# Kernel tuning notes

Hardware: AMD Instinct MI355X
Metric: run time of the kernel (lower is better)

The kernel has to match this reference:

```python
import jax, jax.numpy as jnp
import numpy as np

N = 512      # num_nodes
B = 32       # batch
T = 12       # encoder seq_len
HOR = 12     # decoder horizon
U = 64       # rnn_units
K = 2        # max_diffusion_step
M = 2 * K + 1  # num_matrices (2 supports)


def setup_inputs() -> dict:
    key = jax.random.key(0)
    ks = jax.random.split(key, 16)

    # dual random-walk supports: (D^-1 A)^T and (D^-1 A^T)^T, with self loops
    adj = (jax.random.uniform(ks[0], (N, N)) < 32.0 / N).astype(jnp.float32)

    def rw_T(a):
        a = a + jnp.eye(N, dtype=jnp.float32)
        return (a / a.sum(axis=1, keepdims=True)).T

    supports = jnp.stack([rw_T(adj), rw_T(adj.T)])  # (2, N, N)

    def w(k, shape, s=0.1):
        return jax.random.normal(k, shape, dtype=jnp.float32) * s

    Cin0 = (1 + U) * M   # layer0: input_dim(1)+units, times num_matrices
    Cin1 = (U + U) * M   # layer1
    return {
        "inputs": jax.random.normal(ks[1], (T, B, N * 1), dtype=jnp.float32),
        "supports": supports,
        "enc0_Wg": w(ks[2], (Cin0, 2 * U)), "enc0_bg": jnp.ones(2 * U, jnp.float32),
        "enc0_Wc": w(ks[3], (Cin0, U)),     "enc0_bc": jnp.zeros(U, jnp.float32),
        "enc1_Wg": w(ks[4], (Cin1, 2 * U)), "enc1_bg": jnp.ones(2 * U, jnp.float32),
        "enc1_Wc": w(ks[5], (Cin1, U)),     "enc1_bc": jnp.zeros(U, jnp.float32),
        "dec0_Wg": w(ks[6], (Cin0, 2 * U)), "dec0_bg": jnp.ones(2 * U, jnp.float32),
        "dec0_Wc": w(ks[7], (Cin0, U)),     "dec0_bc": jnp.zeros(U, jnp.float32),
        "dec1_Wg": w(ks[8], (Cin1, 2 * U)), "dec1_bg": jnp.ones(2 * U, jnp.float32),
        "dec1_Wc": w(ks[9], (Cin1, U)),     "dec1_bc": jnp.zeros(U, jnp.float32),
        "proj_W": w(ks[10], (U, 1)),        "proj_b": jnp.zeros(1, jnp.float32),
    }


def reference(inputs, supports, enc0_Wg, enc0_bg, enc0_Wc, enc0_bc,
              enc1_Wg, enc1_bg, enc1_Wc, enc1_bc,
              dec0_Wg, dec0_bg, dec0_Wc, dec0_bc,
              dec1_Wg, dec1_bg, dec1_Wc, dec1_bc, proj_W, proj_b):
    Bsz = inputs.shape[1]

    def gconv(x0, W, b):
        # x0: (B, N, C); Chebyshev-style diffusion over each support
        xs = [x0]
        for i in range(supports.shape[0]):
            s = supports[i]
            x1 = jnp.einsum('ij,bjc->bic', s, x0)
            xs.append(x1)
            xp, xpp = x1, x0
            for _ in range(K - 1):
                x2 = 2.0 * jnp.einsum('ij,bjc->bic', s, xp) - xpp
                xs.append(x2)
                xp, xpp = x2, xp
        # stack on last axis to match torch's (B,N,C,num_matrices) -> (B*N, C*M) layout
        z = jnp.stack(xs, axis=-1).reshape(Bsz, N, -1)
        return z @ W + b

    def cell(x, h, Wg, bg, Wc, bc):
        g = jax.nn.sigmoid(gconv(jnp.concatenate([x, h], axis=-1), Wg, bg))
        r, u = jnp.split(g, 2, axis=-1)
        c = jnp.tanh(gconv(jnp.concatenate([x, r * h], axis=-1), Wc, bc))
        return u * h + (1.0 - u) * c

    h0 = jnp.zeros((Bsz, N, U), inputs.dtype)
    h1 = jnp.zeros((Bsz, N, U), inputs.dtype)

    def enc_step(carry, xt):
        h0, h1 = carry
        x = xt.reshape(Bsz, N, 1)
        h0 = cell(x, h0, enc0_Wg, enc0_bg, enc0_Wc, enc0_bc)
        h1 = cell(h0, h1, enc1_Wg, enc1_bg, enc1_Wc, enc1_bc)
        return (h0, h1), None

    (h0, h1), _ = jax.lax.scan(enc_step, (h0, h1), inputs)

    def dec_step(carry, _):
        h0, h1, xin = carry
        h0 = cell(xin, h0, dec0_Wg, dec0_bg, dec0_Wc, dec0_bc)
        h1 = cell(h0, h1, dec1_Wg, dec1_bg, dec1_Wc, dec1_bc)
        out = h1 @ proj_W + proj_b        # (B, N, 1)
        return (h0, h1, out), out.reshape(Bsz, N)

    go = jnp.zeros((Bsz, N, 1), inputs.dtype)
    _, outs = jax.lax.scan(dec_step, (h0, h1, go), None, length=HOR)
    return outs  # (horizon, B, N*output_dim)
```

## Files before the change

kernel.cpp:

```cpp
#include <hip/hip_runtime.h>
#include <math.h>

#define NN 512
#define BB 32
#define TT 12
#define HH 12
#define UU 64
#define CAP 128
#define RTOT (NN * BB)

__device__ __forceinline__ float sigm(float x) { return 1.f / (1.f + expf(-x)); }

__global__ void zero_kernel(float* __restrict__ p, int n) {
    int i = blockIdx.x * 256 + threadIdx.x;
    if (i < n) p[i] = 0.0f;
}

__global__ __launch_bounds__(256) void row_counts(const float* __restrict__ sup,
                                                  int* __restrict__ cnt) {
    int wave = (blockIdx.x * 256 + threadIdx.x) >> 6;
    int lane = threadIdx.x & 63;
    if (wave >= 2 * NN) return;
    const float* row = sup + (size_t)wave * NN;
    int c = 0;
    for (int k = 0; k < 8; ++k)
        c += __popcll(__ballot(row[k * 64 + lane] != 0.0f));
    if (lane == 0) cnt[wave] = c;
}

__global__ __launch_bounds__(512) void perm_build(const int* __restrict__ cnt,
                                                  int* __restrict__ nmap,
                                                  int* __restrict__ rankv) {
    __shared__ int hist[520];
    __shared__ int keys[512];
    int n = threadIdx.x;
    int c0 = cnt[n], c1 = cnt[NN + n];
    int key = c0 > c1 ? c0 : c1;
    hist[n] = 0;
    if (n < 8) hist[512 + n] = 0;
    __syncthreads();
    keys[n] = key;
    atomicAdd(&hist[key], 1);
    __syncthreads();
    if (n == 0) {
        int s = 0;
        for (int i = 0; i < 520; ++i) { int h = hist[i]; hist[i] = s; s += h; }
    }
    __syncthreads();
    int pos = hist[key];
    for (int i = 0; i < n; ++i)
        if (keys[i] == key) ++pos;
    nmap[pos] = n;
    rankv[n] = pos;
}

__global__ __launch_bounds__(256) void build_ell(const float* __restrict__ sup,
                                                 const int* __restrict__ nmap,
                                                 const int* __restrict__ rankv,
                                                 int2* __restrict__ ell8,
                                                 int2* __restrict__ ell4,
                                                 int* __restrict__ ecnt) {
    int wave = (blockIdx.x * blockDim.x + threadIdx.x) >> 6;
    int lane = threadIdx.x & 63;
    if (wave >= 2 * NN) return;
    int s = wave >> 9, rp = wave & 511;
    const float* row = sup + ((size_t)s * NN + nmap[rp]) * NN;
    int base = 0;
    for (int k = 0; k < NN / 64; ++k) {
        float v = row[k * 64 + lane];
        unsigned long long m = __ballot(v != 0.0f);
        int pre = __popcll(m & ((1ull << lane) - 1ull));
        if (v != 0.0f) {
            int pos = base + pre;
            if (pos < CAP) {
                int j = rankv[k * 64 + lane];
                int vb = __float_as_int(v);
                ell8[(size_t)pos * 1024 + wave] = make_int2(j * 32 + ((j >> 2) & 1) * 16, vb);
                ell4[(size_t)pos * 1024 + wave] = make_int2(j * 16, vb);
            }
        }
        base += __popcll(m);
    }
    if (lane == 0) ecnt[wave] = base < CAP ? base : CAP;
}

__global__ void wmax_kernel(const int* __restrict__ ecnt, int* __restrict__ wmax) {
    int g = threadIdx.x;
    if (g >= 16) return;
    int s = g >> 3, grp = g & 7;
    int m = 0;
    for (int i = 0; i < 64; ++i) {
        int c = ecnt[s * NN + grp * 64 + i];
        m = c > m ? c : m;
    }
    wmax[g] = m;
}

__global__ void wprep(const float* __restrict__ src, float* __restrict__ dstP,
                      float* __restrict__ dstX, int C, int OO, int WD, int L0) {
    int idx = blockIdx.x * 256 + threadIdx.x;
    int total = 5 * C * OO;
    if (idx >= total) return;
    int oi = idx % WD;
    int rem = idx / WD;
    int c = rem % C;
    int rem2 = rem / C;
    int m = rem2 % 5;
    int oq = rem2 / 5;
    int o = oq * WD + oi;
    int crow = L0 ? (c + 1) : c;
    size_t base = (size_t)crow * 5 * OO + o;
    float v;
    if (m == 0) v = src[base] - src[base + 2 * OO] - src[base + 4 * OO];
    else        v = src[base + (size_t)m * OO];
    dstP[idx] = v;
    if (L0 && c == 0) {
        size_t b0 = (size_t)o;
        float xvv;
        if (m == 0) xvv = src[b0] - src[b0 + 2 * OO] - src[b0 + 4 * OO];
        else        xvv = src[b0 + (size_t)m * OO];
        dstX[(oq * 5 + m) * WD + oi] = xvv;
    }
}

template<bool L0, bool GATE>
__global__ __launch_bounds__(512) void fused(const float* __restrict__ hA,
                                             const float* __restrict__ hB,
                                             const float* __restrict__ g,
                                             const float* __restrict__ Wp,
                                             const float* __restrict__ Xr,
                                             const float* __restrict__ xv,
                                             const int* __restrict__ nmap,
                                             const float* __restrict__ bias,
                                             const int2* __restrict__ ell,
                                             const int* __restrict__ wmax,
                                             float* __restrict__ gout,
                                             const float* __restrict__ hOld,
                                             float* __restrict__ hNew) {
    constexpr int C  = L0 ? 64 : 128;
    constexpr int WD = GATE ? 8 : 4;

    __shared__ float S[512 * WD * 2];
    float* T0 = S;
    float* T1 = S + 512 * WD;

    int bid = blockIdx.x;
    int swz = (bid & 7) * 64 + (bid >> 3);
    int b = swz >> 4, oq = swz & 15;
    int o0 = oq * WD;
    int n = threadIdx.x;
    int wm0 = wmax[n >> 6];
    int wm1 = wmax[8 + (n >> 6)];
    float xn = L0 ? xv[b * 512 + nmap[n]] : 0.f;

    const float* Wb = Wp + (size_t)oq * 5 * C * WD;
    float acc[5][WD];
    #pragma unroll
    for (int oi = 0; oi < WD; ++oi) acc[0][oi] = bias[o0 + oi];
    #pragma unroll
    for (int m = 1; m < 5; ++m)
        #pragma unroll
        for (int oi = 0; oi < WD; ++oi) acc[m][oi] = 0.f;

    #pragma unroll 2
    for (int c = 0; c < C; ++c) {
        float a;
        if (L0) {
            if (GATE) a = hA[(size_t)((b << 6) + c) * 512 + n];
            else      a = g[(size_t)((b << 7) + c) * 512 + n];
        } else {
            if (c < 64) {
                a = hA[(size_t)((b << 6) + c) * 512 + n];
            } else {
                int u = c - 64;
                if (GATE) a = hB[(size_t)((b << 6) + u) * 512 + n];
                else      a = g[(size_t)((b << 7) + u) * 512 + n];
            }
        }
        #pragma unroll
        for (int m = 0; m < 5; ++m) {
            const float* wrow = Wb + ((size_t)m * C + c) * WD;
            #pragma unroll
            for (int oi = 0; oi < WD; ++oi)
                acc[m][oi] += a * wrow[oi];
        }
    }

    if (L0) {
        const float* xr = Xr + (size_t)oq * 5 * WD;
        #pragma unroll
        for (int m = 0; m < 5; ++m)
            #pragma unroll
            for (int oi = 0; oi < WD; ++oi)
                acc[m][oi] += xn * xr[m * WD + oi];
    }

    float uval[WD], hval[WD];
    if (!GATE) {
        #pragma unroll
        for (int oi = 0; oi < WD; ++oi) {
            uval[oi] = g[(size_t)((b << 7) + 64 + o0 + oi) * 512 + n];
            hval[oi] = hOld[(size_t)((b << 6) + o0 + oi) * 512 + n];
        }
    }

    int hsel = (n >> 2) & 1;
    if constexpr (WD == 8) {
        *(float4*)&T0[n * 8 + hsel * 4] =
            make_float4(acc[2][0], acc[2][1], acc[2][2], acc[2][3]);
        *(float4*)&T0[n * 8 + (hsel ^ 1) * 4] =
            make_float4(acc[2][4], acc[2][5], acc[2][6], acc[2][7]);
        *(float4*)&T1[n * 8 + hsel * 4] =
            make_float4(acc[4][0], acc[4][1], acc[4][2], acc[4][3]);
        *(float4*)&T1[n * 8 + (hsel ^ 1) * 4] =
            make_float4(acc[4][4], acc[4][5], acc[4][6], acc[4][7]);
    } else {
        *(float4*)&T0[n * 4] = make_float4(acc[2][0], acc[2][1], acc[2][2], acc[2][3]);
        *(float4*)&T1[n * 4] = make_float4(acc[4][0], acc[4][1], acc[4][2], acc[4][3]);
    }

    auto gather = [&](const float* T, const int2* e0, int wm, float* o) {
        const char* Tbyte = (const char*)T;
        float a0[WD];
        #pragma unroll
        for (int i = 0; i < WD; ++i) a0[i] = 0.f;
        #pragma unroll 2
        for (int p = 0; p < wm; ++p) {
            int2 e = e0[(size_t)p << 10];
            float v = __int_as_float(e.y);
            if constexpr (WD == 8) {
                float4 x0 = *(const float4*)(Tbyte + e.x);
                float4 x1 = *(const float4*)(Tbyte + (e.x ^ 16));
                a0[0] += v * x0.x; a0[1] += v * x0.y; a0[2] += v * x0.z; a0[3] += v * x0.w;
                a0[4] += v * x1.x; a0[5] += v * x1.y; a0[6] += v * x1.z; a0[7] += v * x1.w;
            } else {
                float4 x0 = *(const float4*)(Tbyte + e.x);
                a0[0] += v * x0.x; a0[1] += v * x0.y; a0[2] += v * x0.z; a0[3] += v * x0.w;
            }
        }
        #pragma unroll
        for (int i = 0; i < WD; ++i) o[i] = a0[i];
    };
    auto put = [&](float* T, const float* y) {
        if constexpr (WD == 8) {
            *(float4*)&T[n * 8 + hsel * 4]       = make_float4(y[0], y[1], y[2], y[3]);
            *(float4*)&T[n * 8 + (hsel ^ 1) * 4] = make_float4(y[4], y[5], y[6], y[7]);
        } else {
            *(float4*)&T[n * 4] = make_float4(y[0], y[1], y[2], y[3]);
        }
    };

    const int2* e00 = ell + n;
    const int2* e01 = ell + NN + n;
    float g2[WD], g4[WD], t1[WD];

    __syncthreads();

    gather(T0, e00, wm0, t1);
    #pragma unroll
    for (int oi = 0; oi < WD; ++oi) acc[1][oi] += 2.f * t1[oi];
    gather(T1, e01, wm1, t1);
    #pragma unroll
    for (int oi = 0; oi < WD; ++oi) acc[3][oi] += 2.f * t1[oi];

    __syncthreads();

    put(T0, acc[1]);
    put(T1, acc[3]);

    __syncthreads();

    gather(T0, e00, wm0, g2);
    gather(T1, e01, wm1, g4);

    #pragma unroll
    for (int oi = 0; oi < WD; ++oi) {
        float accf = acc[0][oi] + g2[oi] + g4[oi];
        if (GATE) {
            float s = sigm(accf);
            if (oq < 8) {
                const float* hG = L0 ? hA : hB;
                float hv = hG[(size_t)((b << 6) + o0 + oi) * 512 + n];
                gout[(size_t)((b << 7) + o0 + oi) * 512 + n] = s * hv;
            } else {
                gout[(size_t)((b << 7) + o0 + oi) * 512 + n] = s;
            }
        } else {
            float cv = tanhf(accf);
            hNew[(size_t)((b << 6) + o0 + oi) * 512 + n] =
                uval[oi] * hval[oi] + (1.f - uval[oi]) * cv;
        }
    }
}

__global__ void proj_kernel(const float* __restrict__ h1, const float* __restrict__ pW,
                            const float* __restrict__ pb, const int* __restrict__ nmap,
                            float* __restrict__ outt) {
    int r = blockIdx.x * 256 + threadIdx.x;
    if (r >= RTOT) return;
    int b = r >> 9, n = r & 511;
    float acc = pb[0];
    #pragma unroll 16
    for (int u = 0; u < 64; ++u)
        acc += h1[(size_t)((b << 6) + u) * 512 + n] * pW[u];
    outt[b * NN + nmap[n]] = acc;
}

extern "C" void kernel_launch(void* const* d_in, const int* in_sizes, int n_in,
                              void* d_out, int out_size, void* d_ws, size_t ws_size,
                              hipStream_t stream) {
    const float* inputs   = (const float*)d_in[0];
    const float* supports = (const float*)d_in[1];
    const float* enc0_Wg = (const float*)d_in[2];
    const float* enc0_bg = (const float*)d_in[3];
    const float* enc0_Wc = (const float*)d_in[4];
    const float* enc0_bc = (const float*)d_in[5];
    const float* enc1_Wg = (const float*)d_in[6];
    const float* enc1_bg = (const float*)d_in[7];
    const float* enc1_Wc = (const float*)d_in[8];
    const float* enc1_bc = (const float*)d_in[9];
    const float* dec0_Wg = (const float*)d_in[10];
    const float* dec0_bg = (const float*)d_in[11];
    const float* dec0_Wc = (const float*)d_in[12];
    const float* dec0_bc = (const float*)d_in[13];
    const float* dec1_Wg = (const float*)d_in[14];
    const float* dec1_bg = (const float*)d_in[15];
    const float* dec1_Wc = (const float*)d_in[16];
    const float* dec1_bc = (const float*)d_in[17];
    const float* projW   = (const float*)d_in[18];
    const float* projb   = (const float*)d_in[19];
    float* out = (float*)d_out;

    char* wsb = (char*)d_ws;
    size_t off = 0;
    auto alloc = [&](size_t bytes) -> char* {
        char* p = wsb + off;
        off = (off + bytes + 255) & ~(size_t)255;
        return p;
    };
    int2*  ell8  = (int2*)alloc((size_t)CAP * 1024 * 8);
    int2*  ell4  = (int2*)alloc((size_t)CAP * 1024 * 8);
    int*   cnt   = (int*)alloc((size_t)2 * NN * 4);
    int*   nmap  = (int*)alloc((size_t)NN * 4);
    int*   rankv = (int*)alloc((size_t)NN * 4);
    int*   ecnt  = (int*)alloc((size_t)2 * NN * 4);
    int*   wmax  = (int*)alloc((size_t)16 * 4);
    float* h0a   = (float*)alloc((size_t)RTOT * UU * 4);
    float* h1a   = (float*)alloc((size_t)RTOT * UU * 4);
    float* xzero = (float*)alloc((size_t)RTOT * 4);
    float* h0b   = (float*)alloc((size_t)RTOT * UU * 4);
    float* h1b   = (float*)alloc((size_t)RTOT * UU * 4);
    float* g     = (float*)alloc((size_t)RTOT * 128 * 4);
    float* p_e0g = (float*)alloc((size_t)5 * 64 * 128 * 4);
    float* x_e0g = (float*)alloc((size_t)16 * 5 * 8 * 4);
    float* p_e0c = (float*)alloc((size_t)5 * 64 * 64 * 4);
    float* x_e0c = (float*)alloc((size_t)16 * 5 * 4 * 4);
    float* p_e1g = (float*)alloc((size_t)5 * 128 * 128 * 4);
    float* p_e1c = (float*)alloc((size_t)5 * 128 * 64 * 4);
    float* p_d0g = (float*)alloc((size_t)5 * 64 * 128 * 4);
    float* x_d0g = (float*)alloc((size_t)16 * 5 * 8 * 4);
    float* p_d0c = (float*)alloc((size_t)5 * 64 * 64 * 4);
    float* x_d0c = (float*)alloc((size_t)16 * 5 * 4 * 4);
    float* p_d1g = (float*)alloc((size_t)5 * 128 * 128 * 4);
    float* p_d1c = (float*)alloc((size_t)5 * 128 * 64 * 4);
    float* xdum  = (float*)alloc((size_t)16 * 5 * 8 * 4);
    if (off > ws_size) return;

    {
        int nz = CAP * 1024 * 4;
        zero_kernel<<<(nz + 255) / 256, 256, 0, stream>>>((float*)ell8, nz);
    }
    row_counts<<<256, 256, 0, stream>>>(supports, cnt);
    perm_build<<<1, 512, 0, stream>>>(cnt, nmap, rankv);
    build_ell<<<256, 256, 0, stream>>>(supports, nmap, rankv, ell8, ell4, ecnt);
    wmax_kernel<<<1, 16, 0, stream>>>(ecnt, wmax);
    {
        int nz = RTOT * UU * 2 + RTOT;
        zero_kernel<<<(nz + 255) / 256, 256, 0, stream>>>(h0a, nz);
    }
    wprep<<<(5 * 64 * 128 + 255) / 256, 256, 0, stream>>>(enc0_Wg, p_e0g, x_e0g, 64, 128, 8, 1);
    wprep<<<(5 * 64 * 64 + 255) / 256, 256, 0, stream>>>(enc0_Wc, p_e0c, x_e0c, 64, 64, 4, 1);
    wprep<<<(5 * 128 * 128 + 255) / 256, 256, 0, stream>>>(enc1_Wg, p_e1g, xdum, 128, 128, 8, 0);
    wprep<<<(5 * 128 * 64 + 255) / 256, 256, 0, stream>>>(enc1_Wc, p_e1c, xdum, 128, 64, 4, 0);
    wprep<<<(5 * 64 * 128 + 255) / 256, 256, 0, stream>>>(dec0_Wg, p_d0g, x_d0g, 64, 128, 8, 1);
    wprep<<<(5 * 64 * 64 + 255) / 256, 256, 0, stream>>>(dec0_Wc, p_d0c, x_d0c, 64, 64, 4, 1);
    wprep<<<(5 * 128 * 128 + 255) / 256, 256, 0, stream>>>(dec1_Wg, p_d1g, xdum, 128, 128, 8, 0);
    wprep<<<(5 * 128 * 64 + 255) / 256, 256, 0, stream>>>(dec1_Wc, p_d1c, xdum, 128, 64, 4, 0);

    float *h0c = h0a, *h0n = h0b, *h1c = h1a, *h1n = h1b;

    auto cell_l0 = [&](const float* x_bn, const float* Wg_, const float* Xg_,
                       const float* bg_, const float* Wc_, const float* Xc_,
                       const float* bc_) {
        fused<true, true><<<512, 512, 0, stream>>>(h0c, nullptr, g, Wg_, Xg_, x_bn, nmap,
                                                   bg_, ell8, wmax, g, nullptr, nullptr);
        fused<true, false><<<512, 512, 0, stream>>>(h0c, nullptr, g, Wc_, Xc_, x_bn, nmap,
                                                    bc_, ell4, wmax, nullptr, h0c, h0n);
        float* t = h0c; h0c = h0n; h0n = t;
    };
    auto cell_l1 = [&](const float* Wg_, const float* bg_,
                       const float* Wc_, const float* bc_) {
        fused<false, true><<<512, 512, 0, stream>>>(h0c, h1c, g, Wg_, nullptr, nullptr, nmap,
                                                    bg_, ell8, wmax, g, nullptr, nullptr);
        fused<false, false><<<512, 512, 0, stream>>>(h0c, h1c, g, Wc_, nullptr, nullptr, nmap,
                                                     bc_, ell4, wmax, nullptr, h1c, h1n);
        float* t = h1c; h1c = h1n; h1n = t;
    };

    for (int t = 0; t < TT; ++t) {
        cell_l0(inputs + (size_t)t * BB * NN, p_e0g, x_e0g, enc0_bg, p_e0c, x_e0c, enc0_bc);
        cell_l1(p_e1g, enc1_bg, p_e1c, enc1_bc);
    }
    for (int t = 0; t < HH; ++t) {
        const float* xin = (t == 0) ? xzero : (out + (size_t)(t - 1) * BB * NN);
        cell_l0(xin, p_d0g, x_d0g, dec0_bg, p_d0c, x_d0c, dec0_bc);
        cell_l1(p_d1g, dec1_bg, p_d1c, dec1_bc);
        proj_kernel<<<(RTOT + 255) / 256, 256, 0, stream>>>(h1c, projW, projb, nmap,
                                                            out + (size_t)t * BB * NN);
    }
}
```

Measured before the change: 4.652 ms.

## Wavefront-pipeline encoder layers by fusing layer1 step t with layer0 step t+1

```diff
diff --git a/kernel.cpp b/kernel.cpp
--- a/kernel.cpp
+++ b/kernel.cpp
@@ -124,27 +124,26 @@
 }
 
 template<bool L0, bool GATE>
-__global__ __launch_bounds__(512) void fused(const float* __restrict__ hA,
-                                             const float* __restrict__ hB,
-                                             const float* __restrict__ g,
-                                             const float* __restrict__ Wp,
-                                             const float* __restrict__ Xr,
-                                             const float* __restrict__ xv,
-                                             const int* __restrict__ nmap,
-                                             const float* __restrict__ bias,
-                                             const int2* __restrict__ ell,
-                                             const int* __restrict__ wmax,
-                                             float* __restrict__ gout,
-                                             const float* __restrict__ hOld,
-                                             float* __restrict__ hNew) {
+__device__ __forceinline__ void fused_body(int bid, float* __restrict__ S,
+                                           const float* __restrict__ hA,
+                                           const float* __restrict__ hB,
+                                           const float* __restrict__ g,
+                                           const float* __restrict__ Wp,
+                                           const float* __restrict__ Xr,
+                                           const float* __restrict__ xv,
+                                           const int* __restrict__ nmap,
+                                           const float* __restrict__ bias,
+                                           const int2* __restrict__ ell,
+                                           const int* __restrict__ wmax,
+                                           float* __restrict__ gout,
+                                           const float* __restrict__ hOld,
+                                           float* __restrict__ hNew) {
     constexpr int C  = L0 ? 64 : 128;
     constexpr int WD = GATE ? 8 : 4;
 
-    __shared__ float S[512 * WD * 2];
     float* T0 = S;
     float* T1 = S + 512 * WD;
 
-    int bid = blockIdx.x;
     int swz = (bid & 7) * 64 + (bid >> 3);
     int b = swz >> 4, oq = swz & 15;
     int o0 = oq * WD;
@@ -291,6 +290,48 @@
                 uval[oi] * hval[oi] + (1.f - uval[oi]) * cv;
         }
     }
+}
+
+template<bool L0, bool GATE>
+__global__ __launch_bounds__(512) void fused(const float* __restrict__ hA,
+                                             const float* __restrict__ hB,
+                                             const float* __restrict__ g,
+                                             const float* __restrict__ Wp,
+                                             const float* __restrict__ Xr,
+                                             const float* __restrict__ xv,
+                                             const int* __restrict__ nmap,
+                                             const float* __restrict__ bias,
+                                             const int2* __restrict__ ell,
+                                             const int* __restrict__ wmax,
+                                             float* __restrict__ gout,
+                                             const float* __restrict__ hOld,
+                                             float* __restrict__ hNew) {
+    __shared__ float S[512 * (GATE ? 8 : 4) * 2];
+    fused_body<L0, GATE>(blockIdx.x, S, hA, hB, g, Wp, Xr, xv, nmap, bias,
+                         ell, wmax, gout, hOld, hNew);
+}
+
+template<bool GATE>
+__global__ __launch_bounds__(512) void fused_pair(
+        const int* __restrict__ nmap, const int2* __restrict__ ell,
+        const int* __restrict__ wmax,
+        const float* __restrict__ AhA, const float* __restrict__ AhB,
+        const float* __restrict__ Ag,  const float* __restrict__ AWp,
+        const float* __restrict__ Abias, float* __restrict__ Agout,
+        const float* __restrict__ AhOld, float* __restrict__ AhNew,
+        const float* __restrict__ BhA, const float* __restrict__ Bg,
+        const float* __restrict__ BWp, const float* __restrict__ BXr,
+        const float* __restrict__ Bxv, const float* __restrict__ Bbias,
+        float* __restrict__ Bgout, const float* __restrict__ BhOld,
+        float* __restrict__ BhNew) {
+    __shared__ float S[512 * (GATE ? 8 : 4) * 2];
+    int unit = blockIdx.x & 1, sub = blockIdx.x >> 1;
+    if (unit == 0)
+        fused_body<false, GATE>(sub, S, AhA, AhB, Ag, AWp, nullptr, nullptr,
+                                nmap, Abias, ell, wmax, Agout, AhOld, AhNew);
+    else
+        fused_body<true, GATE>(sub, S, BhA, nullptr, Bg, BWp, BXr, Bxv,
+                               nmap, Bbias, ell, wmax, Bgout, BhOld, BhNew);
 }
 
 __global__ void proj_kernel(const float* __restrict__ h1, const float* __restrict__ pW,
@@ -350,7 +391,8 @@
     float* xzero = (float*)alloc((size_t)RTOT * 4);
     float* h0b   = (float*)alloc((size_t)RTOT * UU * 4);
     float* h1b   = (float*)alloc((size_t)RTOT * UU * 4);
-    float* g     = (float*)alloc((size_t)RTOT * 128 * 4);
+    float* g0    = (float*)alloc((size_t)RTOT * 128 * 4);
+    float* g1    = (float*)alloc((size_t)RTOT * 128 * 4);
     float* p_e0g = (float*)alloc((size_t)5 * 64 * 128 * 4);
     float* x_e0g = (float*)alloc((size_t)16 * 5 * 8 * 4);
     float* p_e0c = (float*)alloc((size_t)5 * 64 * 64 * 4);
@@ -392,29 +434,55 @@
     auto cell_l0 = [&](const float* x_bn, const float* Wg_, const float* Xg_,
                        const float* bg_, const float* Wc_, const float* Xc_,
                        const float* bc_) {
-        fused<true, true><<<512, 512, 0, stream>>>(h0c, nullptr, g, Wg_, Xg_, x_bn, nmap,
-                                                   bg_, ell8, wmax, g, nullptr, nullptr);
-        fused<true, false><<<512, 512, 0, stream>>>(h0c, nullptr, g, Wc_, Xc_, x_bn, nmap,
+        fused<true, true><<<512, 512, 0, stream>>>(h0c, nullptr, g0, Wg_, Xg_, x_bn, nmap,
+                                                   bg_, ell8, wmax, g0, nullptr, nullptr);
+        fused<true, false><<<512, 512, 0, stream>>>(h0c, nullptr, g0, Wc_, Xc_, x_bn, nmap,
                                                     bc_, ell4, wmax, nullptr, h0c, h0n);
         float* t = h0c; h0c = h0n; h0n = t;
     };
     auto cell_l1 = [&](const float* Wg_, const float* bg_,
                        const float* Wc_, const float* bc_) {
-        fused<false, true><<<512, 512, 0, stream>>>(h0c, h1c, g, Wg_, nullptr, nullptr, nmap,
-                                                    bg_, ell8, wmax, g, nullptr, nullptr);
-        fused<false, false><<<512, 512, 0, stream>>>(h0c, h1c, g, Wc_, nullptr, nullptr, nmap,
+        fused<false, true><<<512, 512, 0, stream>>>(h0c, h1c, g1, Wg_, nullptr, nullptr, nmap,
+                                                    bg_, ell8, wmax, g1, nullptr, nullptr);
+        fused<false, false><<<512, 512, 0, stream>>>(h0c, h1c, g1, Wc_, nullptr, nullptr, nmap,
                                                      bc_, ell4, wmax, nullptr, h1c, h1n);
         float* t = h1c; h1c = h1n; h1n = t;
     };
-
-    for (int t = 0; t < TT; ++t) {
-        cell_l0(inputs + (size_t)t * BB * NN, p_e0g, x_e0g, enc0_bg, p_e0c, x_e0c, enc0_bc);
-        cell_l1(p_e1g, enc1_bg, p_e1c, enc1_bc);
-    }
-    for (int t = 0; t < HH; ++t) {
-        const float* xin = (t == 0) ? xzero : (out + (size_t)(t - 1) * BB * NN);
+    auto pair_step = [&](const float* xB, const float* BWg, const float* BXg,
+                         const float* Bbg, const float* BWc, const float* BXc,
+                         const float* Bbc) {
+        fused_pair<true><<<1024, 512, 0, stream>>>(
+            nmap, ell8, wmax,
+            h0c, h1c, g1, p_e1g, enc1_bg, g1, nullptr, nullptr,
+            h0c, g0, BWg, BXg, xB, Bbg, g0, nullptr, nullptr);
+        fused_pair<false><<<1024, 512, 0, stream>>>(
+            nmap, ell4, wmax,
+            h0c, h1c, g1, p_e1c, enc1_bc, nullptr, h1c, h1n,
+            h0c, g0, BWc, BXc, xB, Bbc, nullptr, h0c, h0n);
+        float* t = h0c; h0c = h0n; h0n = t;
+        t = h1c; h1c = h1n; h1n = t;
+    };
+
+    cell_l0(inputs, p_e0g, x_e0g, enc0_bg, p_e0c, x_e0c, enc0_bc);
+    for (int t = 1; t < TT; ++t)
+        pair_step(inputs + (size_t)t * BB * NN,
+                  p_e0g, x_e0g, enc0_bg, p_e0c, x_e0c, enc0_bc);
+    pair_step(xzero, p_d0g, x_d0g, dec0_bg, p_d0c, x_d0c, dec0_bc);
+
+    auto cell_l1_dec = [&]() {
+        fused<false, true><<<512, 512, 0, stream>>>(h0c, h1c, g1, p_d1g, nullptr, nullptr, nmap,
+                                                    dec1_bg, ell8, wmax, g1, nullptr, nullptr);
+        fused<false, false><<<512, 512, 0, stream>>>(h0c, h1c, g1, p_d1c, nullptr, nullptr, nmap,
+                                                     dec1_bc, ell4, wmax, nullptr, h1c, h1n);
+        float* t = h1c; h1c = h1n; h1n = t;
+    };
+
+    cell_l1_dec();
+    proj_kernel<<<(RTOT + 255) / 256, 256, 0, stream>>>(h1c, projW, projb, nmap, out);
+    for (int t = 1; t < HH; ++t) {
+        const float* xin = out + (size_t)(t - 1) * BB * NN;
         cell_l0(xin, p_d0g, x_d0g, dec0_bg, p_d0c, x_d0c, dec0_bc);
-        cell_l1(p_d1g, dec1_bg, p_d1c, dec1_bc);
+        cell_l1_dec();
         proj_kernel<<<(RTOT + 255) / 256, 256, 0, stream>>>(h1c, projW, projb, nmap,
                                                             out + (size_t)t * BB * NN);
     }
```

After: 4.908 ms. 5.5% more time.
